# Performance work log

Hardware: AMD Instinct MI355X
Metric: run time of the kernel (lower is better)

## Reference

```python
import jax, jax.numpy as jnp
import numpy as np

N = 20000        # nodes
E = 320000       # edges (avg degree 16)
NHID = 256       # hidden dim (decoder input features)
NFEAT = 256      # reconstructed attribute dim
K_SELECTED = 4096  # number of nodes with label == 1 (static for jit)


def setup_inputs() -> dict:
    key = jax.random.key(0)
    ks = jax.random.split(key, 12)
    feature_attribute = jax.random.normal(ks[0], (N, NHID), dtype=jnp.float32)
    edge_row = jax.random.randint(ks[1], (E,), 0, N, dtype=jnp.int32)
    edge_col = jax.random.randint(ks[2], (E,), 0, N, dtype=jnp.int32)
    # positive, roughly degree-normalized adjacency weights
    edge_w = jax.random.uniform(ks[3], (E,), dtype=jnp.float32) / 16.0
    # first K_SELECTED nodes are labeled 1, rest 0 (static count for jit)
    labels = jnp.concatenate([jnp.ones((K_SELECTED,), jnp.int32),
                              jnp.zeros((N - K_SELECTED,), jnp.int32)])
    stdv1 = 1.0 / np.sqrt(NHID)
    stdv2 = 1.0 / np.sqrt(NFEAT)
    W1_ad = jax.random.uniform(ks[4], (NHID, NHID), minval=-stdv1, maxval=stdv1, dtype=jnp.float32)
    b1_ad = jax.random.uniform(ks[5], (NHID,), minval=-stdv1, maxval=stdv1, dtype=jnp.float32)
    W2_ad = jax.random.uniform(ks[6], (NHID, NFEAT), minval=-stdv2, maxval=stdv2, dtype=jnp.float32)
    b2_ad = jax.random.uniform(ks[7], (NFEAT,), minval=-stdv2, maxval=stdv2, dtype=jnp.float32)
    W_sd = jax.random.uniform(ks[8], (NHID, NHID), minval=-stdv1, maxval=stdv1, dtype=jnp.float32)
    b_sd = jax.random.uniform(ks[9], (NHID,), minval=-stdv1, maxval=stdv1, dtype=jnp.float32)
    return dict(feature_attribute=feature_attribute, edge_row=edge_row, edge_col=edge_col,
                edge_w=edge_w, labels=labels, W1_ad=W1_ad, b1_ad=b1_ad,
                W2_ad=W2_ad, b2_ad=b2_ad, W_sd=W_sd, b_sd=b_sd)


def reference(feature_attribute, edge_row, edge_col, edge_w, labels,
              W1_ad, b1_ad, W2_ad, b2_ad, W_sd, b_sd):
    def gcn(x, W, b):
        support = x @ W                                   # [N, d_out] dense mm
        msg = support[edge_col] * edge_w[:, None]         # gather + scale [E, d_out]
        out = jax.ops.segment_sum(msg, edge_row, num_segments=N)  # spmm aggregation
        return out + b

    # static-size index of labeled nodes (labels==1 count is K_SELECTED)
    idx = jnp.nonzero(labels == 1, size=K_SELECTED)[0]

    # Attribute decoder: relu(gc1) -> (dropout, eval: identity) -> gc2 -> select
    h = jax.nn.relu(gcn(feature_attribute, W1_ad, b1_ad))
    pred_attribute_mat = gcn(h, W2_ad, b2_ad)[idx]        # [K, NFEAT]

    # Structure decoder: gc1 -> select -> x @ x.T
    s = gcn(feature_attribute, W_sd, b_sd)[idx]           # [K, NHID]
    pred_adj_mat = s @ s.T                                # [K, K]

    return pred_attribute_mat, pred_adj_mat
```

## Files before the change

kernel.cpp:

```cpp
#include <hip/hip_runtime.h>
#include <hip/hip_bf16.h>

#define NN   20000
#define NE   320000
#define KSEL 4096

typedef short bf16x8 __attribute__((ext_vector_type(8)));
typedef float f32x4  __attribute__((ext_vector_type(4)));

static __device__ __forceinline__ float bf2f(unsigned short u){
  return __uint_as_float(((unsigned int)u) << 16);
}
static __device__ __forceinline__ unsigned short f2bf(float f){
  unsigned int x = __float_as_uint(f);
  x += 0x7fffu + ((x >> 16) & 1u);
  return (unsigned short)(x >> 16);
}
static __device__ __forceinline__ void gld_lds16(const unsigned short* g, unsigned short* l){
  __builtin_amdgcn_global_load_lds(
      (const __attribute__((address_space(1))) unsigned int*)g,
      (__attribute__((address_space(3))) unsigned int*)l, 16, 0, 0);
}

__global__ __launch_bounds__(256) void k_prep(const float* __restrict__ X,
    const float* __restrict__ W1, const float* __restrict__ Wsd, const float* __restrict__ W2,
    const int* __restrict__ labels,
    unsigned short* __restrict__ Xb, unsigned short* __restrict__ Wt,
    int* __restrict__ counts, int* __restrict__ partA){
  int b = blockIdx.x, tid = threadIdx.x;
  if (b < 5000){
    int i = (b * 256 + tid) * 4;
    float4 v = *(const float4*)(X + i);
    ushort4 o = { f2bf(v.x), f2bf(v.y), f2bf(v.z), f2bf(v.w) };
    *(ushort4*)(Xb + i) = o;
  } else if (b < 5768){
    int t = (b - 5000) * 256 + tid;
    int w = t >> 16, o = (t >> 8) & 255, k = t & 255;
    const float* W = (w == 0) ? W1 : (w == 1 ? Wsd : W2);
    Wt[t] = f2bf(W[k * 256 + o]);
  } else {
    __shared__ int ws[4];
    int z = b - 5768, lane = tid & 63, wv = tid >> 6;
    if (tid < 250) *(int4*)&counts[z * 1000 + tid * 4] = make_int4(0, 0, 0, 0);
    int base = z * 1024 + tid * 4;
    int s = 0;
    #pragma unroll
    for (int j = 0; j < 4; ++j){
      int n0 = base + j;
      if (n0 < NN) s += (labels[n0] == 1) ? 1 : 0;
    }
    #pragma unroll
    for (int off = 32; off; off >>= 1) s += __shfl_down(s, off, 64);
    if (lane == 0) ws[wv] = s;
    __syncthreads();
    if (tid == 0) partA[z] = ws[0] + ws[1] + ws[2] + ws[3];
  }
}

__global__ void k_hist(const int* __restrict__ row, int* __restrict__ counts){
  int e = blockIdx.x * 256 + threadIdx.x;
  if (e < NE) atomicAdd(&counts[row[e]], 1);
}

__global__ __launch_bounds__(256) void k_idx_emit(const int* __restrict__ labels,
    const int* __restrict__ partA, int* __restrict__ idx){
  __shared__ int ws[4];
  __shared__ int boff_s;
  int tid = threadIdx.x, lane = tid & 63, wv = tid >> 6;
  if (tid < 64){
    int v = (lane < 20) ? partA[lane] : 0;
    int acc = v;
    #pragma unroll
    for (int off = 1; off < 32; off <<= 1){
      int t = __shfl_up(acc, off, 64);
      if (lane >= off) acc += t;
    }
    if (lane == (int)blockIdx.x) boff_s = acc - v;
  }
  int base = blockIdx.x * 1024 + tid * 4;
  int c[4]; int s = 0;
  #pragma unroll
  for (int j = 0; j < 4; ++j){
    int n0 = base + j;
    c[j] = (n0 < NN && labels[n0] == 1) ? 1 : 0;
    s += c[j];
  }
  int incl = s;
  #pragma unroll
  for (int off = 1; off < 64; off <<= 1){
    int t = __shfl_up(incl, off, 64);
    if (lane >= off) incl += t;
  }
  if (lane == 63) ws[wv] = incl;
  __syncthreads();
  int woff = boff_s;
  for (int w = 0; w < wv; ++w) woff += ws[w];
  int off = woff + incl - s;
  #pragma unroll
  for (int j = 0; j < 4; ++j){
    if (c[j]){ if (off < KSEL) idx[off] = base + j; ++off; }
  }
}

__global__ __launch_bounds__(256) void k_row_emit(const int* __restrict__ counts,
    int* __restrict__ start, int* __restrict__ cursor){
  __shared__ int ws[4];
  __shared__ int red[4];
  int tid = threadIdx.x, lane = tid & 63, wv = tid >> 6;
  int base = blockIdx.x * 1024;
  int ps = 0;
  for (int i = tid * 4; i < base; i += 1024){
    int4 v = *(const int4*)&counts[i];
    ps += v.x + v.y + v.z + v.w;
  }
  #pragma unroll
  for (int off = 32; off; off >>= 1) ps += __shfl_down(ps, off, 64);
  if (lane == 0) red[wv] = ps;
  __syncthreads();
  int bpref = red[0] + red[1] + red[2] + red[3];
  int nb = base + tid * 4;
  int c[4]; int s = 0;
  #pragma unroll
  for (int j = 0; j < 4; ++j){
    int n0 = nb + j;
    c[j] = (n0 < NN) ? counts[n0] : 0;
    s += c[j];
  }
  int incl = s;
  #pragma unroll
  for (int off = 1; off < 64; off <<= 1){
    int t = __shfl_up(incl, off, 64);
    if (lane >= off) incl += t;
  }
  if (lane == 63) ws[wv] = incl;
  __syncthreads();
  int woff = bpref;
  for (int w = 0; w < wv; ++w) woff += ws[w];
  int run = woff + incl - s;
  #pragma unroll
  for (int j = 0; j < 4; ++j){
    int n0 = nb + j;
    if (n0 < NN){ start[n0] = run; cursor[n0] = run; run += c[j]; }
  }
  if (blockIdx.x == 0 && tid == 0) start[NN] = NE;
}

__global__ void k_scatter(const int* __restrict__ row, const int* __restrict__ col,
                          const float* __restrict__ ew, int* __restrict__ cursor,
                          int2* __restrict__ rec){
  int e = blockIdx.x * 256 + threadIdx.x;
  if (e < NE){
    int r = row[e];
    int p = atomicAdd(&cursor[r], 1);
    rec[p] = make_int2(col[e], __float_as_int(ew[e]));
  }
}

__global__ __launch_bounds__(256) void k_spmm_full(const unsigned short* __restrict__ Xb,
    const int* __restrict__ start, const int2* __restrict__ rec,
    unsigned short* __restrict__ aggX){
  int wave = threadIdx.x >> 6, lane = threadIdx.x & 63;
  int n = blockIdx.x * 4 + wave;
  int s = start[n], e = start[n + 1];
  int d = lane * 4;
  float a0 = 0, a1 = 0, a2 = 0, a3 = 0;
  for (int base = s; base < e; base += 64){
    int p = base + lane;
    int pc = p < e ? p : e - 1;
    int2 r = rec[pc];
    float wv = (p < e) ? __int_as_float(r.y) : 0.0f;
    int m = e - base; if (m > 64) m = 64;
    for (int j = 0; j < m; j += 4){
      int   c0 = __shfl(r.x, j),     c1 = __shfl(r.x, j + 1);
      int   c2 = __shfl(r.x, j + 2), c3 = __shfl(r.x, j + 3);
      float w0 = __shfl(wv, j),      w1 = __shfl(wv, j + 1);
      float w2 = __shfl(wv, j + 2),  w3 = __shfl(wv, j + 3);
      ushort4 v0 = *(const ushort4*)&Xb[(size_t)c0 * 256 + d];
      ushort4 v1 = *(const ushort4*)&Xb[(size_t)c1 * 256 + d];
      ushort4 v2 = *(const ushort4*)&Xb[(size_t)c2 * 256 + d];
      ushort4 v3 = *(const ushort4*)&Xb[(size_t)c3 * 256 + d];
      a0 += w0 * bf2f(v0.x) + w1 * bf2f(v1.x) + w2 * bf2f(v2.x) + w3 * bf2f(v3.x);
      a1 += w0 * bf2f(v0.y) + w1 * bf2f(v1.y) + w2 * bf2f(v2.y) + w3 * bf2f(v3.y);
      a2 += w0 * bf2f(v0.z) + w1 * bf2f(v1.z) + w2 * bf2f(v2.z) + w3 * bf2f(v3.z);
      a3 += w0 * bf2f(v0.w) + w1 * bf2f(v1.w) + w2 * bf2f(v2.w) + w3 * bf2f(v3.w);
    }
  }
  ushort4 o = { f2bf(a0), f2bf(a1), f2bf(a2), f2bf(a3) };
  *(ushort4*)&aggX[(size_t)n * 256 + d] = o;
}

__global__ __launch_bounds__(256) void k_gemm_h(const unsigned short* __restrict__ A,
                                                const unsigned short* __restrict__ Wt,
                                                const float* __restrict__ bias,
                                                unsigned short* __restrict__ out, int M){
  __shared__ unsigned short At[128 * 64];
  __shared__ unsigned short Bt[64 * 64];
  int tid = threadIdx.x, wave = tid >> 6, lane = tid & 63;
  int lm = lane & 15, lq = lane >> 4;
  int mBase = blockIdx.x * 128;
  int oBase = blockIdx.y * 64;
  f32x4 acc[2][4] = {};
  for (int kc = 0; kc < 256; kc += 64){
    if (kc) __syncthreads();
    #pragma unroll
    for (int it = 0; it < 4; ++it){
      int s = (wave * 4 + it) * 64 + lane;
      int row = s >> 3, c = (s & 7) ^ (row & 7);
      int gr = mBase + row; if (gr >= M) gr = M - 1;
      gld_lds16(&A[(size_t)gr * 256 + kc + c * 8], &At[s * 8]);
    }
    #pragma unroll
    for (int it = 0; it < 2; ++it){
      int s = (wave * 2 + it) * 64 + lane;
      int row = s >> 3, c = (s & 7) ^ (row & 7);
      gld_lds16(&Wt[(size_t)(oBase + row) * 256 + kc + c * 8], &Bt[s * 8]);
    }
    __syncthreads();
    #pragma unroll
    for (int ks = 0; ks < 64; ks += 32){
      int cb = ks >> 3;
      int RA = wave * 32 + lm;
      int ca = ((cb + lq) ^ (RA & 7)) << 3;
      bf16x8 a0 = *(const bf16x8*)&At[RA * 64 + ca];
      bf16x8 a1 = *(const bf16x8*)&At[(RA + 16) * 64 + ca];
      #pragma unroll
      for (int os = 0; os < 4; ++os){
        int RB = os * 16 + lm;
        bf16x8 b = *(const bf16x8*)&Bt[RB * 64 + (((cb + lq) ^ (RB & 7)) << 3)];
        acc[0][os] = __builtin_amdgcn_mfma_f32_16x16x32_bf16(a0, b, acc[0][os], 0, 0, 0);
        acc[1][os] = __builtin_amdgcn_mfma_f32_16x16x32_bf16(a1, b, acc[1][os], 0, 0, 0);
      }
    }
  }
  #pragma unroll
  for (int ms = 0; ms < 2; ++ms){
    int rb = mBase + wave * 32 + ms * 16 + lq * 4;
    #pragma unroll
    for (int os = 0; os < 4; ++os){
      int col = oBase + os * 16 + lm;
      float bv = bias[col];
      #pragma unroll
      for (int r = 0; r < 4; ++r){
        int row = rb + r;
        if (row < M) out[(size_t)row * 256 + col] = f2bf(fmaxf(acc[ms][os][r] + bv, 0.f));
      }
    }
  }
}

__global__ __launch_bounds__(256) void k_spmm_selH(const unsigned short* __restrict__ h,
    const int* __restrict__ idx, const int* __restrict__ start, const int2* __restrict__ rec,
    unsigned short* __restrict__ aggH){
  int wave = threadIdx.x >> 6, lane = threadIdx.x & 63;
  int i = blockIdx.x * 4 + wave;
  int n = idx[i];
  int s = start[n], e = start[n + 1];
  int d = lane * 4;
  float a0 = 0, a1 = 0, a2 = 0, a3 = 0;
  for (int base = s; base < e; base += 64){
    int p = base + lane;
    int pc = p < e ? p : e - 1;
    int2 r = rec[pc];
    float wv = (p < e) ? __int_as_float(r.y) : 0.0f;
    int m = e - base; if (m > 64) m = 64;
    for (int j = 0; j < m; j += 4){
      int   c0 = __shfl(r.x, j),     c1 = __shfl(r.x, j + 1);
      int   c2 = __shfl(r.x, j + 2), c3 = __shfl(r.x, j + 3);
      float w0 = __shfl(wv, j),      w1 = __shfl(wv, j + 1);
      float w2 = __shfl(wv, j + 2),  w3 = __shfl(wv, j + 3);
      ushort4 v0 = *(const ushort4*)&h[(size_t)c0 * 256 + d];
      ushort4 v1 = *(const ushort4*)&h[(size_t)c1 * 256 + d];
      ushort4 v2 = *(const ushort4*)&h[(size_t)c2 * 256 + d];
      ushort4 v3 = *(const ushort4*)&h[(size_t)c3 * 256 + d];
      a0 += w0 * bf2f(v0.x) + w1 * bf2f(v1.x) + w2 * bf2f(v2.x) + w3 * bf2f(v3.x);
      a1 += w0 * bf2f(v0.y) + w1 * bf2f(v1.y) + w2 * bf2f(v2.y) + w3 * bf2f(v3.y);
      a2 += w0 * bf2f(v0.z) + w1 * bf2f(v1.z) + w2 * bf2f(v2.z) + w3 * bf2f(v3.z);
      a3 += w0 * bf2f(v0.w) + w1 * bf2f(v1.w) + w2 * bf2f(v2.w) + w3 * bf2f(v3.w);
    }
  }
  ushort4 o = { f2bf(a0), f2bf(a1), f2bf(a2), f2bf(a3) };
  *(ushort4*)&aggH[(size_t)i * 256 + d] = o;
}

__global__ __launch_bounds__(256) void k_gemm_os(const unsigned short* __restrict__ aggH,
    const unsigned short* __restrict__ aggX, const int* __restrict__ idx,
    const unsigned short* __restrict__ Wt,
    const float* __restrict__ b2, const float* __restrict__ bsd,
    float* __restrict__ out0, unsigned short* __restrict__ sel){
  __shared__ unsigned short lds[64 * 264];
  int tid = threadIdx.x;
  int wave = tid >> 6, lane = tid & 63;
  int lm = lane & 15, lq = lane >> 4;
  int z = blockIdx.z;
  int mBase = blockIdx.x * 128;
  int oBase = blockIdx.y * 64;
  const unsigned short* Wt2 = Wt + (z ? 256 * 256 : 512 * 256);
  const float* bias = z ? bsd : b2;
  #pragma unroll
  for (int it = 0; it < 8; ++it){
    int c = it * 256 + tid;
    int o = c >> 5, kk = (c & 31) << 3;
    *(bf16x8*)&lds[o * 264 + kk] = *(const bf16x8*)&Wt2[(oBase + o) * 256 + kk];
  }
  __syncthreads();
  int r0 = mBase + wave * 32 + lm;
  const unsigned short* A0;
  const unsigned short* A1;
  if (z){
    A0 = aggX + (size_t)idx[r0] * 256;
    A1 = aggX + (size_t)idx[r0 + 16] * 256;
  } else {
    A0 = aggH + (size_t)r0 * 256;
    A1 = aggH + (size_t)(r0 + 16) * 256;
  }
  f32x4 acc[2][4] = {};
  #pragma unroll
  for (int ks = 0; ks < 256; ks += 32){
    int ka = ks + lq * 8;
    bf16x8 a0 = *(const bf16x8*)&A0[ka];
    bf16x8 a1 = *(const bf16x8*)&A1[ka];
    #pragma unroll
    for (int os = 0; os < 4; ++os){
      bf16x8 b = *(const bf16x8*)&lds[(os * 16 + lm) * 264 + ka];
      acc[0][os] = __builtin_amdgcn_mfma_f32_16x16x32_bf16(a0, b, acc[0][os], 0, 0, 0);
      acc[1][os] = __builtin_amdgcn_mfma_f32_16x16x32_bf16(a1, b, acc[1][os], 0, 0, 0);
    }
  }
  #pragma unroll
  for (int ms = 0; ms < 2; ++ms){
    int rb = mBase + wave * 32 + ms * 16 + lq * 4;
    #pragma unroll
    for (int os = 0; os < 4; ++os){
      int col = oBase + os * 16 + lm;
      float bv = bias[col];
      #pragma unroll
      for (int r = 0; r < 4; ++r){
        float v = acc[ms][os][r] + bv;
        if (z) sel[(size_t)(rb + r) * 256 + col] = f2bf(v);
        else   out0[(size_t)(rb + r) * 256 + col] = v;
      }
    }
  }
}

__global__ __launch_bounds__(256) void k_gemm_st(const unsigned short* __restrict__ S,
                                                 float* __restrict__ out1){
  __shared__ unsigned short At[128 * 64];
  __shared__ unsigned short Bt[128 * 64];
  int tid = threadIdx.x, wave = tid >> 6, lane = tid & 63;
  int lm = lane & 15, lq = lane >> 4;
  int mBase = blockIdx.x * 128;
  int oBase = blockIdx.y * 128;
  f32x4 acc[2][8] = {};
  for (int kc = 0; kc < 256; kc += 64){
    if (kc) __syncthreads();
    #pragma unroll
    for (int it = 0; it < 4; ++it){
      int s = (wave * 4 + it) * 64 + lane;
      int row = s >> 3, c = (s & 7) ^ (row & 7);
      gld_lds16(&S[(size_t)(mBase + row) * 256 + kc + c * 8], &At[s * 8]);
      gld_lds16(&S[(size_t)(oBase + row) * 256 + kc + c * 8], &Bt[s * 8]);
    }
    __syncthreads();
    #pragma unroll
    for (int ks = 0; ks < 64; ks += 32){
      int cb = ks >> 3;
      int RA = wave * 32 + lm;
      int ca = ((cb + lq) ^ (RA & 7)) << 3;
      bf16x8 a0 = *(const bf16x8*)&At[RA * 64 + ca];
      bf16x8 a1 = *(const bf16x8*)&At[(RA + 16) * 64 + ca];
      #pragma unroll
      for (int os = 0; os < 8; ++os){
        int RB = os * 16 + lm;
        bf16x8 b = *(const bf16x8*)&Bt[RB * 64 + (((cb + lq) ^ (RB & 7)) << 3)];
        acc[0][os] = __builtin_amdgcn_mfma_f32_16x16x32_bf16(a0, b, acc[0][os], 0, 0, 0);
        acc[1][os] = __builtin_amdgcn_mfma_f32_16x16x32_bf16(a1, b, acc[1][os], 0, 0, 0);
      }
    }
  }
  #pragma unroll
  for (int ms = 0; ms < 2; ++ms){
    int rb = mBase + wave * 32 + ms * 16 + lq * 4;
    #pragma unroll
    for (int os = 0; os < 8; ++os){
      int col = oBase + os * 16 + lm;
      #pragma unroll
      for (int r = 0; r < 4; ++r)
        out1[(size_t)(rb + r) * 4096 + col] = acc[ms][os][r];
    }
  }
}

extern "C" void kernel_launch(void* const* d_in, const int* in_sizes, int n_in,
                              void* d_out, int out_size, void* d_ws, size_t ws_size,
                              hipStream_t stream){
  const float* X    = (const float*)d_in[0];
  const int*   erow = (const int*)d_in[1];
  const int*   ecol = (const int*)d_in[2];
  const float* ew   = (const float*)d_in[3];
  const int*   labels = (const int*)d_in[4];
  const float* W1   = (const float*)d_in[5];
  const float* b1   = (const float*)d_in[6];
  const float* W2   = (const float*)d_in[7];
  const float* b2   = (const float*)d_in[8];
  const float* Wsd  = (const float*)d_in[9];
  const float* bsd  = (const float*)d_in[10];
  float* out0 = (float*)d_out;
  float* out1 = out0 + (size_t)KSEL * 256;

  char* ws = (char*)d_ws;
  unsigned short* Xb   = (unsigned short*)(ws);
  unsigned short* Wt   = (unsigned short*)(ws + 10240000);
  unsigned short* aggX = (unsigned short*)(ws + 10633216);
  unsigned short* h    = (unsigned short*)(ws + 20873216);
  unsigned short* aggH = (unsigned short*)(ws + 31113216);
  unsigned short* sel  = (unsigned short*)(ws + 33210368);
  int* idx    = (int*)(ws + 35307520);
  int* counts = (int*)(ws + 35323904);
  int* startp = (int*)(ws + 35403904);
  int* cursor = (int*)(ws + 35483908);
  int2* rec   = (int2*)(ws + 35563912);
  int* partA  = (int*)(ws + 38123912);

  k_prep<<<5788, 256, 0, stream>>>(X, W1, Wsd, W2, labels, Xb, Wt, counts, partA);
  k_hist<<<NE / 256, 256, 0, stream>>>(erow, counts);
  k_idx_emit<<<20, 256, 0, stream>>>(labels, partA, idx);
  k_row_emit<<<20, 256, 0, stream>>>(counts, startp, cursor);
  k_scatter<<<NE / 256, 256, 0, stream>>>(erow, ecol, ew, cursor, rec);
  k_spmm_full<<<5000, 256, 0, stream>>>(Xb, startp, rec, aggX);
  k_gemm_h<<<dim3(157, 4), 256, 0, stream>>>(aggX, Wt, b1, h, NN);
  k_spmm_selH<<<1024, 256, 0, stream>>>(h, idx, startp, rec, aggH);
  k_gemm_os<<<dim3(32, 4, 2), 256, 0, stream>>>(aggH, aggX, idx, Wt, b2, bsd, out0, sel);
  k_gemm_st<<<dim3(32, 32), 256, 0, stream>>>(sel, out1);
}
```

Before: 208.1 us.

## Widen loads to 16 bytes, tile weight transpose, merge hist/idx kernels

The bf16 conversion of X now handles 8 elements per thread with 16-byte stores. The weight transpose goes through an LDS tile so both its global reads and writes are coalesced, replacing the strided per-element gather. The histogram and index-emission kernels are merged into one launch. Both SpMM kernels use 16-byte gathers with each half-wave taking alternate edges, then combine the halves by a shuffle before the store. This cuts launches and memory transactions, at the cost of extra shuffles and twice the accumulator registers per lane.

```diff
diff --git a/kernel.cpp b/kernel.cpp
--- a/kernel.cpp
+++ b/kernel.cpp
@@ -28,19 +28,38 @@
     unsigned short* __restrict__ Xb, unsigned short* __restrict__ Wt,
     int* __restrict__ counts, int* __restrict__ partA){
   int b = blockIdx.x, tid = threadIdx.x;
-  if (b < 5000){
-    int i = (b * 256 + tid) * 4;
-    float4 v = *(const float4*)(X + i);
-    ushort4 o = { f2bf(v.x), f2bf(v.y), f2bf(v.z), f2bf(v.w) };
-    *(ushort4*)(Xb + i) = o;
-  } else if (b < 5768){
-    int t = (b - 5000) * 256 + tid;
-    int w = t >> 16, o = (t >> 8) & 255, k = t & 255;
+  if (b < 2500){
+    int i = (b * 256 + tid) * 8;
+    float4 v0 = *(const float4*)(X + i);
+    float4 v1 = *(const float4*)(X + i + 4);
+    bf16x8 o;
+    o[0] = (short)f2bf(v0.x); o[1] = (short)f2bf(v0.y);
+    o[2] = (short)f2bf(v0.z); o[3] = (short)f2bf(v0.w);
+    o[4] = (short)f2bf(v1.x); o[5] = (short)f2bf(v1.y);
+    o[6] = (short)f2bf(v1.z); o[7] = (short)f2bf(v1.w);
+    *(bf16x8*)(Xb + i) = o;
+  } else if (b < 2548){
+    __shared__ unsigned short lt[64 * 65];
+    int b2 = b - 2500;
+    int w = b2 >> 4, t = b2 & 15;
+    int tR = (t >> 2) * 64, tC = (t & 3) * 64;
     const float* W = (w == 0) ? W1 : (w == 1 ? Wsd : W2);
-    Wt[t] = f2bf(W[k * 256 + o]);
+    #pragma unroll
+    for (int it = 0; it < 16; ++it){
+      int lin = it * 256 + tid;
+      int r = lin >> 6, c = lin & 63;
+      lt[c * 65 + r] = f2bf(W[(size_t)(tR + r) * 256 + tC + c]);
+    }
+    __syncthreads();
+    #pragma unroll
+    for (int it = 0; it < 16; ++it){
+      int lin = it * 256 + tid;
+      int o = lin >> 6, k = lin & 63;
+      Wt[(size_t)w * 65536 + (size_t)(tC + o) * 256 + tR + k] = lt[o * 65 + k];
+    }
   } else {
     __shared__ int ws[4];
-    int z = b - 5768, lane = tid & 63, wv = tid >> 6;
+    int z = b - 2548, lane = tid & 63, wv = tid >> 6;
     if (tid < 250) *(int4*)&counts[z * 1000 + tid * 4] = make_int4(0, 0, 0, 0);
     int base = z * 1024 + tid * 4;
     int s = 0;
@@ -57,16 +76,19 @@
   }
 }
 
-__global__ void k_hist(const int* __restrict__ row, int* __restrict__ counts){
-  int e = blockIdx.x * 256 + threadIdx.x;
-  if (e < NE) atomicAdd(&counts[row[e]], 1);
-}
-
-__global__ __launch_bounds__(256) void k_idx_emit(const int* __restrict__ labels,
-    const int* __restrict__ partA, int* __restrict__ idx){
+__global__ __launch_bounds__(256) void k_hist_idx(const int* __restrict__ row,
+    const int* __restrict__ labels, const int* __restrict__ partA,
+    int* __restrict__ counts, int* __restrict__ idx){
+  int tid = threadIdx.x;
+  if (blockIdx.x < 1250){
+    int e = blockIdx.x * 256 + tid;
+    atomicAdd(&counts[row[e]], 1);
+    return;
+  }
   __shared__ int ws[4];
   __shared__ int boff_s;
-  int tid = threadIdx.x, lane = tid & 63, wv = tid >> 6;
+  int bx = blockIdx.x - 1250;
+  int lane = tid & 63, wv = tid >> 6;
   if (tid < 64){
     int v = (lane < 20) ? partA[lane] : 0;
     int acc = v;
@@ -75,9 +97,9 @@
       int t = __shfl_up(acc, off, 64);
       if (lane >= off) acc += t;
     }
-    if (lane == (int)blockIdx.x) boff_s = acc - v;
-  }
-  int base = blockIdx.x * 1024 + tid * 4;
+    if (lane == bx) boff_s = acc - v;
+  }
+  int base = bx * 1024 + tid * 4;
   int c[4]; int s = 0;
   #pragma unroll
   for (int j = 0; j < 4; ++j){
@@ -160,33 +182,45 @@
     const int* __restrict__ start, const int2* __restrict__ rec,
     unsigned short* __restrict__ aggX){
   int wave = threadIdx.x >> 6, lane = threadIdx.x & 63;
+  int half = lane >> 5, hl = lane & 31;
   int n = blockIdx.x * 4 + wave;
   int s = start[n], e = start[n + 1];
-  int d = lane * 4;
-  float a0 = 0, a1 = 0, a2 = 0, a3 = 0;
+  int d = hl * 8;
+  float acc[8] = {};
   for (int base = s; base < e; base += 64){
     int p = base + lane;
     int pc = p < e ? p : e - 1;
     int2 r = rec[pc];
     float wv = (p < e) ? __int_as_float(r.y) : 0.0f;
     int m = e - base; if (m > 64) m = 64;
-    for (int j = 0; j < m; j += 4){
-      int   c0 = __shfl(r.x, j),     c1 = __shfl(r.x, j + 1);
-      int   c2 = __shfl(r.x, j + 2), c3 = __shfl(r.x, j + 3);
-      float w0 = __shfl(wv, j),      w1 = __shfl(wv, j + 1);
-      float w2 = __shfl(wv, j + 2),  w3 = __shfl(wv, j + 3);
-      ushort4 v0 = *(const ushort4*)&Xb[(size_t)c0 * 256 + d];
-      ushort4 v1 = *(const ushort4*)&Xb[(size_t)c1 * 256 + d];
-      ushort4 v2 = *(const ushort4*)&Xb[(size_t)c2 * 256 + d];
-      ushort4 v3 = *(const ushort4*)&Xb[(size_t)c3 * 256 + d];
-      a0 += w0 * bf2f(v0.x) + w1 * bf2f(v1.x) + w2 * bf2f(v2.x) + w3 * bf2f(v3.x);
-      a1 += w0 * bf2f(v0.y) + w1 * bf2f(v1.y) + w2 * bf2f(v2.y) + w3 * bf2f(v3.y);
-      a2 += w0 * bf2f(v0.z) + w1 * bf2f(v1.z) + w2 * bf2f(v2.z) + w3 * bf2f(v3.z);
-      a3 += w0 * bf2f(v0.w) + w1 * bf2f(v1.w) + w2 * bf2f(v2.w) + w3 * bf2f(v3.w);
-    }
-  }
-  ushort4 o = { f2bf(a0), f2bf(a1), f2bf(a2), f2bf(a3) };
-  *(ushort4*)&aggX[(size_t)n * 256 + d] = o;
+    for (int j = 0; j < m; j += 8){
+      int j0 = j + half, j1 = j + 2 + half, j2 = j + 4 + half, j3 = j + 6 + half;
+      int   c0 = __shfl(r.x, j0), c1 = __shfl(r.x, j1);
+      int   c2 = __shfl(r.x, j2), c3 = __shfl(r.x, j3);
+      float w0 = __shfl(wv, j0),  w1 = __shfl(wv, j1);
+      float w2 = __shfl(wv, j2),  w3 = __shfl(wv, j3);
+      bf16x8 v0 = *(const bf16x8*)&Xb[(size_t)c0 * 256 + d];
+      bf16x8 v1 = *(const bf16x8*)&Xb[(size_t)c1 * 256 + d];
+      bf16x8 v2 = *(const bf16x8*)&Xb[(size_t)c2 * 256 + d];
+      bf16x8 v3 = *(const bf16x8*)&Xb[(size_t)c3 * 256 + d];
+      #pragma unroll
+      for (int q = 0; q < 8; ++q){
+        acc[q] += w0 * bf2f((unsigned short)v0[q]) + w1 * bf2f((unsigned short)v1[q])
+                + w2 * bf2f((unsigned short)v2[q]) + w3 * bf2f((unsigned short)v3[q]);
+      }
+    }
+  }
+  #pragma unroll
+  for (int q = 0; q < 8; ++q){
+    float o = __shfl(acc[q], hl + 32);
+    acc[q] += o;
+  }
+  if (half == 0){
+    bf16x8 ob;
+    #pragma unroll
+    for (int q = 0; q < 8; ++q) ob[q] = (short)f2bf(acc[q]);
+    *(bf16x8*)&aggX[(size_t)n * 256 + d] = ob;
+  }
 }
 
 __global__ __launch_bounds__(256) void k_gemm_h(const unsigned short* __restrict__ A,
@@ -252,34 +286,46 @@
     const int* __restrict__ idx, const int* __restrict__ start, const int2* __restrict__ rec,
     unsigned short* __restrict__ aggH){
   int wave = threadIdx.x >> 6, lane = threadIdx.x & 63;
+  int half = lane >> 5, hl = lane & 31;
   int i = blockIdx.x * 4 + wave;
   int n = idx[i];
   int s = start[n], e = start[n + 1];
-  int d = lane * 4;
-  float a0 = 0, a1 = 0, a2 = 0, a3 = 0;
+  int d = hl * 8;
+  float acc[8] = {};
   for (int base = s; base < e; base += 64){
     int p = base + lane;
     int pc = p < e ? p : e - 1;
     int2 r = rec[pc];
     float wv = (p < e) ? __int_as_float(r.y) : 0.0f;
     int m = e - base; if (m > 64) m = 64;
-    for (int j = 0; j < m; j += 4){
-      int   c0 = __shfl(r.x, j),     c1 = __shfl(r.x, j + 1);
-      int   c2 = __shfl(r.x, j + 2), c3 = __shfl(r.x, j + 3);
-      float w0 = __shfl(wv, j),      w1 = __shfl(wv, j + 1);
-      float w2 = __shfl(wv, j + 2),  w3 = __shfl(wv, j + 3);
-      ushort4 v0 = *(const ushort4*)&h[(size_t)c0 * 256 + d];
-      ushort4 v1 = *(const ushort4*)&h[(size_t)c1 * 256 + d];
-      ushort4 v2 = *(const ushort4*)&h[(size_t)c2 * 256 + d];
-      ushort4 v3 = *(const ushort4*)&h[(size_t)c3 * 256 + d];
-      a0 += w0 * bf2f(v0.x) + w1 * bf2f(v1.x) + w2 * bf2f(v2.x) + w3 * bf2f(v3.x);
-      a1 += w0 * bf2f(v0.y) + w1 * bf2f(v1.y) + w2 * bf2f(v2.y) + w3 * bf2f(v3.y);
-      a2 += w0 * bf2f(v0.z) + w1 * bf2f(v1.z) + w2 * bf2f(v2.z) + w3 * bf2f(v3.z);
-      a3 += w0 * bf2f(v0.w) + w1 * bf2f(v1.w) + w2 * bf2f(v2.w) + w3 * bf2f(v3.w);
-    }
-  }
-  ushort4 o = { f2bf(a0), f2bf(a1), f2bf(a2), f2bf(a3) };
-  *(ushort4*)&aggH[(size_t)i * 256 + d] = o;
+    for (int j = 0; j < m; j += 8){
+      int j0 = j + half, j1 = j + 2 + half, j2 = j + 4 + half, j3 = j + 6 + half;
+      int   c0 = __shfl(r.x, j0), c1 = __shfl(r.x, j1);
+      int   c2 = __shfl(r.x, j2), c3 = __shfl(r.x, j3);
+      float w0 = __shfl(wv, j0),  w1 = __shfl(wv, j1);
+      float w2 = __shfl(wv, j2),  w3 = __shfl(wv, j3);
+      bf16x8 v0 = *(const bf16x8*)&h[(size_t)c0 * 256 + d];
+      bf16x8 v1 = *(const bf16x8*)&h[(size_t)c1 * 256 + d];
+      bf16x8 v2 = *(const bf16x8*)&h[(size_t)c2 * 256 + d];
+      bf16x8 v3 = *(const bf16x8*)&h[(size_t)c3 * 256 + d];
+      #pragma unroll
+      for (int q = 0; q < 8; ++q){
+        acc[q] += w0 * bf2f((unsigned short)v0[q]) + w1 * bf2f((unsigned short)v1[q])
+                + w2 * bf2f((unsigned short)v2[q]) + w3 * bf2f((unsigned short)v3[q]);
+      }
+    }
+  }
+  #pragma unroll
+  for (int q = 0; q < 8; ++q){
+    float o = __shfl(acc[q], hl + 32);
+    acc[q] += o;
+  }
+  if (half == 0){
+    bf16x8 ob;
+    #pragma unroll
+    for (int q = 0; q < 8; ++q) ob[q] = (short)f2bf(acc[q]);
+    *(bf16x8*)&aggH[(size_t)i * 256 + d] = ob;
+  }
 }
 
 __global__ __launch_bounds__(256) void k_gemm_os(const unsigned short* __restrict__ aggH,
@@ -422,9 +468,8 @@
   int2* rec   = (int2*)(ws + 35563912);
   int* partA  = (int*)(ws + 38123912);
 
-  k_prep<<<5788, 256, 0, stream>>>(X, W1, Wsd, W2, labels, Xb, Wt, counts, partA);
-  k_hist<<<NE / 256, 256, 0, stream>>>(erow, counts);
-  k_idx_emit<<<20, 256, 0, stream>>>(labels, partA, idx);
+  k_prep<<<2568, 256, 0, stream>>>(X, W1, Wsd, W2, labels, Xb, Wt, counts, partA);
+  k_hist_idx<<<1270, 256, 0, stream>>>(erow, labels, partA, counts, idx);
   k_row_emit<<<20, 256, 0, stream>>>(counts, startp, cursor);
   k_scatter<<<NE / 256, 256, 0, stream>>>(erow, ecol, ew, cursor, rec);
   k_spmm_full<<<5000, 256, 0, stream>>>(Xb, startp, rec, aggX);
```

Result: no change. 205.2 us (-1.4%).
